# Performance work log

Hardware: AMD Instinct MI355X
Metric: run time of the kernel (lower is better)

The kernel has to match this reference:

```python
import jax, jax.numpy as jnp
import numpy as np

TEMPERATURE = 8.0  # sqrt(d_k), d_k = 64
B, L, D = 32, 2048, 64


def setup_inputs() -> dict:
    key = jax.random.key(0)
    kq, kk, kv, kd, km = jax.random.split(key, 5)
    q = jax.random.normal(kq, (B, L, D), dtype=jnp.float32)
    k = jax.random.normal(kk, (B, L, D), dtype=jnp.float32)
    v = jax.random.normal(kv, (B, L, D), dtype=jnp.float32)
    diag_mask = jax.random.randint(kd, (B, L, L), 0, 2, dtype=jnp.int32)
    mask = jax.random.randint(km, (B, L, L), 0, 2).astype(jnp.bool_)
    return {"q": q, "k": k, "v": v, "diag_mask": diag_mask, "mask": mask}


def reference(q, k, v, diag_mask, mask):
    # attn = (q @ k^T) / temperature              [B, L, L]
    attn = jnp.einsum("bqd,bkd->bqk", q, k) / TEMPERATURE
    # optional mask: masked_fill(mask, -inf)
    attn = jnp.where(mask, -jnp.inf, attn)
    # diag mask: masked_fill(diag_mask == 0, -1e32)
    attn = jnp.where(diag_mask == 0, jnp.float32(-1e32), attn)
    attn = jax.nn.softmax(attn, axis=-1)
    # output = attn @ v                            [B, L, D]
    output = jnp.einsum("bqk,bkd->bqd", attn, v)
    return (output, attn)
```

## Files before the change

kernel.cpp:

```cpp
#include <hip/hip_runtime.h>
#include <cstdint>
#include <cstddef>

#define BB 32
#define LL 2048
#define DD 64

#define BIG_NEG (-3.0e38f)

__global__ __launch_bounds__(256) void k_scores(
    const float* __restrict__ q, const float* __restrict__ kmat,
    const int* __restrict__ diag, const int* __restrict__ mask,
    float* __restrict__ attn)
{
    __shared__ __align__(16) float sQT[32][132];
    __shared__ __align__(16) float sKT[32][132];

    const int b  = blockIdx.z;
    const int q0 = blockIdx.y * 128;
    const int k0 = blockIdx.x * 128;
    const int t  = threadIdx.x;
    const int tx = t & 15;
    const int ty = t >> 4;

    const float* qb = q    + ((size_t)b * LL + q0) * DD;
    const float* kb = kmat + ((size_t)b * LL + k0) * DD;

    float acc[8][8];
    #pragma unroll
    for (int i = 0; i < 8; ++i)
        #pragma unroll
        for (int j = 0; j < 8; ++j) acc[i][j] = 0.0f;

    for (int dc = 0; dc < DD; dc += 32) {
        #pragma unroll
        for (int i = 0; i < 4; ++i) {
            int lin = t + 256 * i;
            int row = lin >> 3;
            int dv  = lin & 7;
            float4 a = *(const float4*)(qb + (size_t)row * DD + dc + dv * 4);
            sQT[dv * 4 + 0][row] = a.x;
            sQT[dv * 4 + 1][row] = a.y;
            sQT[dv * 4 + 2][row] = a.z;
            sQT[dv * 4 + 3][row] = a.w;
            float4 c = *(const float4*)(kb + (size_t)row * DD + dc + dv * 4);
            sKT[dv * 4 + 0][row] = c.x;
            sKT[dv * 4 + 1][row] = c.y;
            sKT[dv * 4 + 2][row] = c.z;
            sKT[dv * 4 + 3][row] = c.w;
        }
        __syncthreads();

        #pragma unroll 8
        for (int d = 0; d < 32; ++d) {
            float4 a0 = *(const float4*)&sQT[d][ty * 8];
            float4 a1 = *(const float4*)&sQT[d][ty * 8 + 4];
            float4 b0 = *(const float4*)&sKT[d][tx * 8];
            float4 b1 = *(const float4*)&sKT[d][tx * 8 + 4];
            float aa[8] = {a0.x, a0.y, a0.z, a0.w, a1.x, a1.y, a1.z, a1.w};
            float bb[8] = {b0.x, b0.y, b0.z, b0.w, b1.x, b1.y, b1.z, b1.w};
            #pragma unroll
            for (int ri = 0; ri < 8; ++ri)
                #pragma unroll
                for (int ci = 0; ci < 8; ++ci)
                    acc[ri][ci] = fmaf(aa[ri], bb[ci], acc[ri][ci]);
        }
        __syncthreads();
    }

    #pragma unroll
    for (int ri = 0; ri < 8; ++ri) {
        int qq = q0 + ty * 8 + ri;
        size_t base = ((size_t)b * LL + qq) * LL + (size_t)(k0 + tx * 8);
        int4 dm0 = *(const int4*)(diag + base);
        int4 dm1 = *(const int4*)(diag + base + 4);
        int4 mk0 = *(const int4*)(mask + base);
        int4 mk1 = *(const int4*)(mask + base + 4);
        int dmv[8] = {dm0.x, dm0.y, dm0.z, dm0.w, dm1.x, dm1.y, dm1.z, dm1.w};
        int mkv[8] = {mk0.x, mk0.y, mk0.z, mk0.w, mk1.x, mk1.y, mk1.z, mk1.w};
        float o[8];
        #pragma unroll
        for (int ci = 0; ci < 8; ++ci) {
            float s = acc[ri][ci] * 0.125f;
            o[ci] = (dmv[ci] == 0 || mkv[ci] != 0) ? BIG_NEG : s;
        }
        *(float4*)(attn + base)     = make_float4(o[0], o[1], o[2], o[3]);
        *(float4*)(attn + base + 4) = make_float4(o[4], o[5], o[6], o[7]);
    }
}

__global__ __launch_bounds__(256) void k_softmax(float* __restrict__ attn)
{
    __shared__ float redm[4];
    __shared__ float reds[4];
    float* p = attn + (size_t)blockIdx.x * LL;
    const int t = threadIdx.x;
    const int wave = t >> 6, lane = t & 63;

    float4 x0 = ((const float4*)p)[t];
    float4 x1 = ((const float4*)p)[t + 256];

    float m = fmaxf(fmaxf(fmaxf(x0.x, x0.y), fmaxf(x0.z, x0.w)),
                    fmaxf(fmaxf(x1.x, x1.y), fmaxf(x1.z, x1.w)));
    #pragma unroll
    for (int off = 32; off >= 1; off >>= 1)
        m = fmaxf(m, __shfl_xor(m, off, 64));
    if (lane == 0) redm[wave] = m;
    __syncthreads();
    m = fmaxf(fmaxf(redm[0], redm[1]), fmaxf(redm[2], redm[3]));

    x0.x = expf(x0.x - m); x0.y = expf(x0.y - m);
    x0.z = expf(x0.z - m); x0.w = expf(x0.w - m);
    x1.x = expf(x1.x - m); x1.y = expf(x1.y - m);
    x1.z = expf(x1.z - m); x1.w = expf(x1.w - m);

    float s = (x0.x + x0.y + x0.z + x0.w) + (x1.x + x1.y + x1.z + x1.w);
    #pragma unroll
    for (int off = 32; off >= 1; off >>= 1)
        s += __shfl_xor(s, off, 64);
    if (lane == 0) reds[wave] = s;
    __syncthreads();
    s = (reds[0] + reds[1]) + (reds[2] + reds[3]);

    float inv = 1.0f / s;
    x0.x *= inv; x0.y *= inv; x0.z *= inv; x0.w *= inv;
    x1.x *= inv; x1.y *= inv; x1.z *= inv; x1.w *= inv;
    ((float4*)p)[t]       = x0;
    ((float4*)p)[t + 256] = x1;
}

__global__ __launch_bounds__(256) void k_pv(
    const float* __restrict__ attn, const float* __restrict__ v,
    float* __restrict__ out)
{
    __shared__ __align__(16) float sPT[64][132];
    __shared__ __align__(16) float sV[64][68];

    const int b  = blockIdx.y;
    const int q0 = blockIdx.x * 128;
    const int t  = threadIdx.x;
    const int tx = t & 15;
    const int ty = t >> 4;

    const float* pb = attn + ((size_t)b * LL + q0) * LL;
    const float* vb = v + (size_t)b * LL * DD;

    float acc[8][4];
    #pragma unroll
    for (int i = 0; i < 8; ++i)
        #pragma unroll
        for (int j = 0; j < 4; ++j) acc[i][j] = 0.0f;

    for (int k0 = 0; k0 < LL; k0 += 64) {
        #pragma unroll
        for (int i = 0; i < 8; ++i) {
            int lin = t + 256 * i;
            int row = lin >> 4;
            int kv  = lin & 15;
            float4 a = *(const float4*)(pb + (size_t)row * LL + k0 + kv * 4);
            sPT[kv * 4 + 0][row] = a.x;
            sPT[kv * 4 + 1][row] = a.y;
            sPT[kv * 4 + 2][row] = a.z;
            sPT[kv * 4 + 3][row] = a.w;
        }
        #pragma unroll
        for (int i = 0; i < 4; ++i) {
            int lin = t + 256 * i;
            int row = lin >> 4;
            int dv  = lin & 15;
            *(float4*)&sV[row][dv * 4] =
                *(const float4*)(vb + (size_t)(k0 + row) * DD + dv * 4);
        }
        __syncthreads();

        #pragma unroll 8
        for (int kk = 0; kk < 64; ++kk) {
            float4 a0 = *(const float4*)&sPT[kk][ty * 8];
            float4 a1 = *(const float4*)&sPT[kk][ty * 8 + 4];
            float4 b0 = *(const float4*)&sV[kk][tx * 4];
            float aa[8] = {a0.x, a0.y, a0.z, a0.w, a1.x, a1.y, a1.z, a1.w};
            float bb[4] = {b0.x, b0.y, b0.z, b0.w};
            #pragma unroll
            for (int ri = 0; ri < 8; ++ri)
                #pragma unroll
                for (int ci = 0; ci < 4; ++ci)
                    acc[ri][ci] = fmaf(aa[ri], bb[ci], acc[ri][ci]);
        }
        __syncthreads();
    }

    #pragma unroll
    for (int ri = 0; ri < 8; ++ri) {
        float4 o = make_float4(acc[ri][0], acc[ri][1], acc[ri][2], acc[ri][3]);
        *(float4*)(out + ((size_t)b * LL + q0 + ty * 8 + ri) * DD + tx * 4) = o;
    }
}

extern "C" void kernel_launch(void* const* d_in, const int* in_sizes, int n_in,
                              void* d_out, int out_size, void* d_ws, size_t ws_size,
                              hipStream_t stream)
{
    const float* q    = (const float*)d_in[0];
    const float* k    = (const float*)d_in[1];
    const float* v    = (const float*)d_in[2];
    const int*   diag = (const int*)d_in[3];
    const int*   mask = (const int*)d_in[4];

    float* out  = (float*)d_out;
    float* attn = out + (size_t)BB * LL * DD;

    k_scores <<<dim3(LL / 128, LL / 128, BB), 256, 0, stream>>>(q, k, diag, mask, attn);
    k_softmax<<<dim3(BB * LL),                256, 0, stream>>>(attn);
    k_pv     <<<dim3(LL / 128, BB),           256, 0, stream>>>(attn, v, out);
}
```

Baseline: 1.685 ms.

## Fuse scores, exp and PV into one bf16 MFMA kernel with post-normalization

```diff
diff --git a/kernel.cpp b/kernel.cpp
--- a/kernel.cpp
+++ b/kernel.cpp
@@ -6,114 +6,142 @@
 #define LL 2048
 #define DD 64
 
-#define BIG_NEG (-3.0e38f)
+typedef __attribute__((ext_vector_type(8))) short bf16x8;
+typedef __attribute__((ext_vector_type(4))) float f32x4;
 
-__global__ __launch_bounds__(256) void k_scores(
+__device__ inline unsigned short f2bf(float x) {
+    union { float f; unsigned u; } v; v.f = x;
+    unsigned r = v.u + 0x7FFFu + ((v.u >> 16) & 1u);
+    return (unsigned short)(r >> 16);
+}
+
+__global__ __launch_bounds__(256) void k_fused(
     const float* __restrict__ q, const float* __restrict__ kmat,
-    const int* __restrict__ diag, const int* __restrict__ mask,
-    float* __restrict__ attn)
+    const float* __restrict__ v, const int* __restrict__ diag,
+    const int* __restrict__ mask, float* __restrict__ attn,
+    float* __restrict__ out)
 {
-    __shared__ __align__(16) float sQT[32][132];
-    __shared__ __align__(16) float sKT[32][132];
+    __shared__ __align__(16) unsigned short sQ[128][72];
+    __shared__ __align__(16) unsigned short sK[64][72];
+    __shared__ __align__(16) unsigned short sVT[64][72];
+    __shared__ __align__(16) unsigned short sP[128][72];
 
-    const int b  = blockIdx.z;
-    const int q0 = blockIdx.y * 128;
-    const int k0 = blockIdx.x * 128;
-    const int t  = threadIdx.x;
-    const int tx = t & 15;
-    const int ty = t >> 4;
+    const int b    = blockIdx.y;
+    const int q0   = blockIdx.x * 128;
+    const int t    = threadIdx.x;
+    const int w    = t >> 6;
+    const int lane = t & 63;
+    const int lr   = lane & 15;
+    const int quad = lane >> 4;
+    const int m0   = w * 32;
 
-    const float* qb = q    + ((size_t)b * LL + q0) * DD;
-    const float* kb = kmat + ((size_t)b * LL + k0) * DD;
+    const float* qb = q + ((size_t)(b * LL + q0)) * DD;
+    #pragma unroll
+    for (int i = 0; i < 8; ++i) {
+        int lin = t + 256 * i;
+        int row = lin >> 4, dv = lin & 15;
+        float4 a = *(const float4*)(qb + (size_t)row * DD + dv * 4);
+        unsigned short* dst = &sQ[row][dv * 4];
+        dst[0] = f2bf(a.x * 0.125f); dst[1] = f2bf(a.y * 0.125f);
+        dst[2] = f2bf(a.z * 0.125f); dst[3] = f2bf(a.w * 0.125f);
+    }
 
-    float acc[8][8];
+    f32x4 O[2][4];
     #pragma unroll
-    for (int i = 0; i < 8; ++i)
+    for (int mi = 0; mi < 2; ++mi)
         #pragma unroll
-        for (int j = 0; j < 8; ++j) acc[i][j] = 0.0f;
+        for (int di = 0; di < 4; ++di) O[mi][di] = (f32x4){0.f, 0.f, 0.f, 0.f};
 
-    for (int dc = 0; dc < DD; dc += 32) {
+    const float* kb = kmat + (size_t)b * LL * DD;
+    const float* vb = v    + (size_t)b * LL * DD;
+
+    for (int k0 = 0; k0 < LL; k0 += 64) {
         #pragma unroll
         for (int i = 0; i < 4; ++i) {
             int lin = t + 256 * i;
-            int row = lin >> 3;
-            int dv  = lin & 7;
-            float4 a = *(const float4*)(qb + (size_t)row * DD + dc + dv * 4);
-            sQT[dv * 4 + 0][row] = a.x;
-            sQT[dv * 4 + 1][row] = a.y;
-            sQT[dv * 4 + 2][row] = a.z;
-            sQT[dv * 4 + 3][row] = a.w;
-            float4 c = *(const float4*)(kb + (size_t)row * DD + dc + dv * 4);
-            sKT[dv * 4 + 0][row] = c.x;
-            sKT[dv * 4 + 1][row] = c.y;
-            sKT[dv * 4 + 2][row] = c.z;
-            sKT[dv * 4 + 3][row] = c.w;
+            int row = lin >> 4, dv = lin & 15;
+            float4 a = *(const float4*)(kb + (size_t)(k0 + row) * DD + dv * 4);
+            unsigned short* dst = &sK[row][dv * 4];
+            dst[0] = f2bf(a.x); dst[1] = f2bf(a.y);
+            dst[2] = f2bf(a.z); dst[3] = f2bf(a.w);
+            float4 c = *(const float4*)(vb + (size_t)(k0 + row) * DD + dv * 4);
+            sVT[dv * 4 + 0][row] = f2bf(c.x);
+            sVT[dv * 4 + 1][row] = f2bf(c.y);
+            sVT[dv * 4 + 2][row] = f2bf(c.z);
+            sVT[dv * 4 + 3][row] = f2bf(c.w);
         }
         __syncthreads();
 
-        #pragma unroll 8
-        for (int d = 0; d < 32; ++d) {
-            float4 a0 = *(const float4*)&sQT[d][ty * 8];
-            float4 a1 = *(const float4*)&sQT[d][ty * 8 + 4];
-            float4 b0 = *(const float4*)&sKT[d][tx * 8];
-            float4 b1 = *(const float4*)&sKT[d][tx * 8 + 4];
-            float aa[8] = {a0.x, a0.y, a0.z, a0.w, a1.x, a1.y, a1.z, a1.w};
-            float bb[8] = {b0.x, b0.y, b0.z, b0.w, b1.x, b1.y, b1.z, b1.w};
+        f32x4 S[2][4];
+        #pragma unroll
+        for (int mi = 0; mi < 2; ++mi)
             #pragma unroll
-            for (int ri = 0; ri < 8; ++ri)
+            for (int ni = 0; ni < 4; ++ni) S[mi][ni] = (f32x4){0.f, 0.f, 0.f, 0.f};
+        #pragma unroll
+        for (int dc = 0; dc < 2; ++dc) {
+            bf16x8 a0 = *(const bf16x8*)&sQ[m0 +      lr][dc * 32 + quad * 8];
+            bf16x8 a1 = *(const bf16x8*)&sQ[m0 + 16 + lr][dc * 32 + quad * 8];
+            #pragma unroll
+            for (int ni = 0; ni < 4; ++ni) {
+                bf16x8 bk = *(const bf16x8*)&sK[ni * 16 + lr][dc * 32 + quad * 8];
+                S[0][ni] = __builtin_amdgcn_mfma_f32_16x16x32_bf16(a0, bk, S[0][ni], 0, 0, 0);
+                S[1][ni] = __builtin_amdgcn_mfma_f32_16x16x32_bf16(a1, bk, S[1][ni], 0, 0, 0);
+            }
+        }
+
+        #pragma unroll
+        for (int mi = 0; mi < 2; ++mi) {
+            int rbase = m0 + mi * 16 + quad * 4;
+            #pragma unroll
+            for (int ni = 0; ni < 4; ++ni) {
+                int gcol = k0 + ni * 16 + lr;
+                size_t idx = ((size_t)(b * LL + q0 + rbase)) * LL + gcol;
                 #pragma unroll
-                for (int ci = 0; ci < 8; ++ci)
-                    acc[ri][ci] = fmaf(aa[ri], bb[ci], acc[ri][ci]);
+                for (int reg = 0; reg < 4; ++reg) {
+                    int dm = diag[idx];
+                    int mk = mask[idx];
+                    float p = (dm == 0 || mk != 0) ? 0.0f : __expf(S[mi][ni][reg]);
+                    attn[idx] = p;
+                    sP[rbase + reg][ni * 16 + lr] = f2bf(p);
+                    idx += LL;
+                }
+            }
+        }
+
+        #pragma unroll
+        for (int kc = 0; kc < 2; ++kc) {
+            bf16x8 a0 = *(const bf16x8*)&sP[m0 +      lr][kc * 32 + quad * 8];
+            bf16x8 a1 = *(const bf16x8*)&sP[m0 + 16 + lr][kc * 32 + quad * 8];
+            #pragma unroll
+            for (int di = 0; di < 4; ++di) {
+                bf16x8 bv = *(const bf16x8*)&sVT[di * 16 + lr][kc * 32 + quad * 8];
+                O[0][di] = __builtin_amdgcn_mfma_f32_16x16x32_bf16(a0, bv, O[0][di], 0, 0, 0);
+                O[1][di] = __builtin_amdgcn_mfma_f32_16x16x32_bf16(a1, bv, O[1][di], 0, 0, 0);
+            }
         }
         __syncthreads();
     }
 
     #pragma unroll
-    for (int ri = 0; ri < 8; ++ri) {
-        int qq = q0 + ty * 8 + ri;
-        size_t base = ((size_t)b * LL + qq) * LL + (size_t)(k0 + tx * 8);
-        int4 dm0 = *(const int4*)(diag + base);
-        int4 dm1 = *(const int4*)(diag + base + 4);
-        int4 mk0 = *(const int4*)(mask + base);
-        int4 mk1 = *(const int4*)(mask + base + 4);
-        int dmv[8] = {dm0.x, dm0.y, dm0.z, dm0.w, dm1.x, dm1.y, dm1.z, dm1.w};
-        int mkv[8] = {mk0.x, mk0.y, mk0.z, mk0.w, mk1.x, mk1.y, mk1.z, mk1.w};
-        float o[8];
+    for (int mi = 0; mi < 2; ++mi)
         #pragma unroll
-        for (int ci = 0; ci < 8; ++ci) {
-            float s = acc[ri][ci] * 0.125f;
-            o[ci] = (dmv[ci] == 0 || mkv[ci] != 0) ? BIG_NEG : s;
-        }
-        *(float4*)(attn + base)     = make_float4(o[0], o[1], o[2], o[3]);
-        *(float4*)(attn + base + 4) = make_float4(o[4], o[5], o[6], o[7]);
-    }
+        for (int di = 0; di < 4; ++di)
+            #pragma unroll
+            for (int reg = 0; reg < 4; ++reg)
+                out[((size_t)(b * LL + q0 + m0 + mi * 16 + quad * 4 + reg)) * DD
+                    + di * 16 + lr] = O[mi][di][reg];
 }
 
-__global__ __launch_bounds__(256) void k_softmax(float* __restrict__ attn)
+__global__ __launch_bounds__(256) void k_norm(
+    float* __restrict__ attn, float* __restrict__ out)
 {
-    __shared__ float redm[4];
     __shared__ float reds[4];
-    float* p = attn + (size_t)blockIdx.x * LL;
-    const int t = threadIdx.x;
-    const int wave = t >> 6, lane = t & 63;
+    const size_t row = blockIdx.x;
+    float* p = attn + row * LL;
+    const int t = threadIdx.x, wave = t >> 6, lane = t & 63;
 
     float4 x0 = ((const float4*)p)[t];
     float4 x1 = ((const float4*)p)[t + 256];
-
-    float m = fmaxf(fmaxf(fmaxf(x0.x, x0.y), fmaxf(x0.z, x0.w)),
-                    fmaxf(fmaxf(x1.x, x1.y), fmaxf(x1.z, x1.w)));
-    #pragma unroll
-    for (int off = 32; off >= 1; off >>= 1)
-        m = fmaxf(m, __shfl_xor(m, off, 64));
-    if (lane == 0) redm[wave] = m;
-    __syncthreads();
-    m = fmaxf(fmaxf(redm[0], redm[1]), fmaxf(redm[2], redm[3]));
-
-    x0.x = expf(x0.x - m); x0.y = expf(x0.y - m);
-    x0.z = expf(x0.z - m); x0.w = expf(x0.w - m);
-    x1.x = expf(x1.x - m); x1.y = expf(x1.y - m);
-    x1.z = expf(x1.z - m); x1.w = expf(x1.w - m);
-
     float s = (x0.x + x0.y + x0.z + x0.w) + (x1.x + x1.y + x1.z + x1.w);
     #pragma unroll
     for (int off = 32; off >= 1; off >>= 1)
@@ -122,77 +150,16 @@
     __syncthreads();
     s = (reds[0] + reds[1]) + (reds[2] + reds[3]);
 
-    float inv = 1.0f / s;
+    const float inv = 1.0f / s;
     x0.x *= inv; x0.y *= inv; x0.z *= inv; x0.w *= inv;
     x1.x *= inv; x1.y *= inv; x1.z *= inv; x1.w *= inv;
     ((float4*)p)[t]       = x0;
     ((float4*)p)[t + 256] = x1;
-}
 
-__global__ __launch_bounds__(256) void k_pv(
-    const float* __restrict__ attn, const float* __restrict__ v,
-    float* __restrict__ out)
-{
-    __shared__ __align__(16) float sPT[64][132];
-    __shared__ __align__(16) float sV[64][68];
-
-    const int b  = blockIdx.y;
-    const int q0 = blockIdx.x * 128;
-    const int t  = threadIdx.x;
-    const int tx = t & 15;
-    const int ty = t >> 4;
-
-    const float* pb = attn + ((size_t)b * LL + q0) * LL;
-    const float* vb = v + (size_t)b * LL * DD;
-
-    float acc[8][4];
-    #pragma unroll
-    for (int i = 0; i < 8; ++i)
-        #pragma unroll
-        for (int j = 0; j < 4; ++j) acc[i][j] = 0.0f;
-
-    for (int k0 = 0; k0 < LL; k0 += 64) {
-        #pragma unroll
-        for (int i = 0; i < 8; ++i) {
-            int lin = t + 256 * i;
-            int row = lin >> 4;
-            int kv  = lin & 15;
-            float4 a = *(const float4*)(pb + (size_t)row * LL + k0 + kv * 4);
-            sPT[kv * 4 + 0][row] = a.x;
-            sPT[kv * 4 + 1][row] = a.y;
-            sPT[kv * 4 + 2][row] = a.z;
-            sPT[kv * 4 + 3][row] = a.w;
-        }
-        #pragma unroll
-        for (int i = 0; i < 4; ++i) {
-            int lin = t + 256 * i;
-            int row = lin >> 4;
-            int dv  = lin & 15;
-            *(float4*)&sV[row][dv * 4] =
-                *(const float4*)(vb + (size_t)(k0 + row) * DD + dv * 4);
-        }
-        __syncthreads();
-
-        #pragma unroll 8
-        for (int kk = 0; kk < 64; ++kk) {
-            float4 a0 = *(const float4*)&sPT[kk][ty * 8];
-            float4 a1 = *(const float4*)&sPT[kk][ty * 8 + 4];
-            float4 b0 = *(const float4*)&sV[kk][tx * 4];
-            float aa[8] = {a0.x, a0.y, a0.z, a0.w, a1.x, a1.y, a1.z, a1.w};
-            float bb[4] = {b0.x, b0.y, b0.z, b0.w};
-            #pragma unroll
-            for (int ri = 0; ri < 8; ++ri)
-                #pragma unroll
-                for (int ci = 0; ci < 4; ++ci)
-                    acc[ri][ci] = fmaf(aa[ri], bb[ci], acc[ri][ci]);
-        }
-        __syncthreads();
-    }
-
-    #pragma unroll
-    for (int ri = 0; ri < 8; ++ri) {
-        float4 o = make_float4(acc[ri][0], acc[ri][1], acc[ri][2], acc[ri][3]);
-        *(float4*)(out + ((size_t)b * LL + q0 + ty * 8 + ri) * DD + tx * 4) = o;
+    if (t < 16) {
+        float4 o = ((float4*)(out + row * DD))[t];
+        o.x *= inv; o.y *= inv; o.z *= inv; o.w *= inv;
+        ((float4*)(out + row * DD))[t] = o;
     }
 }
 
@@ -209,7 +176,6 @@
     float* out  = (float*)d_out;
     float* attn = out + (size_t)BB * LL * DD;
 
-    k_scores <<<dim3(LL / 128, LL / 128, BB), 256, 0, stream>>>(q, k, diag, mask, attn);
-    k_softmax<<<dim3(BB * LL),                256, 0, stream>>>(attn);
-    k_pv     <<<dim3(LL / 128, BB),           256, 0, stream>>>(attn, v, out);
+    k_fused<<<dim3(LL / 128, BB), 256, 0, stream>>>(q, k, v, diag, mask, attn, out);
+    k_norm <<<dim3(BB * LL),      256, 0, stream>>>(attn, out);
 }
```

Result: slower. 1.869 ms (+10.9%).
